# Optimization experiments

Measured on AMD Instinct MI355X. Metric: run time of the kernel, lower is better.

## Reference

```python
import jax, jax.numpy as jnp
import numpy as np

D_MODEL = 768
NUM_HEADS = 12
D_HEAD = D_MODEL // NUM_HEADS
LN_EPS = 1e-5


def layer_norm(x, w, b):
    m = jnp.mean(x, axis=-1, keepdims=True)
    v = jnp.mean(jnp.square(x - m), axis=-1, keepdims=True)
    return (x - m) * jax.lax.rsqrt(v + LN_EPS) * w + b


def setup_inputs() -> dict:
    key = jax.random.key(0)
    ks = jax.random.split(key, 10)
    B, P, NQ, D = 16, 197, 8, D_MODEL
    s = 1.0 / np.sqrt(D)
    return {
        "q_x": jax.random.normal(ks[0], (1, NQ, D), jnp.float32),
        "kv_x": jax.random.normal(ks[1], (B, P, D), jnp.float32),
        "pair_pos_embedding": jax.random.normal(ks[2], (2 * P, D), jnp.float32) * 0.02,
        "q_w": jax.random.normal(ks[3], (D, D), jnp.float32) * s,
        "q_b": jnp.zeros((D,), jnp.float32),
        "kv_w": jax.random.normal(ks[4], (D, D), jnp.float32) * s,
        "kv_b": jnp.zeros((D,), jnp.float32),
        "out_w": jax.random.normal(ks[5], (D, D), jnp.float32) * s,
        "out_b": jnp.zeros((D,), jnp.float32),
        "lnq_w": jnp.ones((D,), jnp.float32),
        "lnq_b": jnp.zeros((D,), jnp.float32),
        "lnkv_w": jnp.ones((D,), jnp.float32),
        "lnkv_b": jnp.zeros((D,), jnp.float32),
    }


def reference(q_x, kv_x, pair_pos_embedding, q_w, q_b, kv_w, kv_b,
              out_w, out_b, lnq_w, lnq_b, lnkv_w, lnkv_b):
    H, dh = NUM_HEADS, D_HEAD
    scale = dh ** -0.5
    _, NQ, D = q_x.shape
    B, P, _ = kv_x.shape

    # q path: Linear -> LN -> split heads -> [1, H, NQ, dh]
    q = layer_norm(q_x @ q_w.T + q_b, lnq_w, lnq_b)
    q = q.reshape(1, NQ, H, dh).transpose(0, 2, 1, 3)  # [1,H,NQ,dh]

    # kv path: Linear -> LN -> split heads -> [B, H, P, dh]
    kv = layer_norm(kv_x @ kv_w.T + kv_b, lnkv_w, lnkv_b)
    kv = kv.reshape(B, P, H, dh).transpose(0, 2, 1, 3)  # [B,H,P,dh]

    # pairwise expansion: kv_concat[i*B+j] = cat(kv[i], kv[j]) along token dim
    kv_rep = jnp.repeat(kv, B, axis=0)          # [B^2,H,P,dh] (repeat_interleave)
    kv_til = jnp.tile(kv, (B, 1, 1, 1))         # [B^2,H,P,dh]
    kv_cat = jnp.concatenate([kv_rep, kv_til], axis=2)  # [B^2,H,2P,dh]

    # positional bias: [2P, D] -> [1, H, 2P, dh]
    pos = pair_pos_embedding.reshape(1, 2 * P, H, dh).transpose(0, 2, 1, 3)
    kv_cat = kv_cat + pos

    scores = jnp.einsum('bhqd,bhpd->bhqp', jnp.broadcast_to(q, (B * B, H, NQ, dh)), kv_cat) * scale
    attn = jax.nn.softmax(scores, axis=-1)      # [B^2,H,NQ,2P]

    v1 = jnp.einsum('bhqp,bhpd->bhqd', attn[..., :P], kv_cat[:, :, :P, :])
    v2 = jnp.einsum('bhqp,bhpd->bhqd', attn[..., P:], kv_cat[:, :, P:, :])
    values = (v1 - v2).transpose(0, 2, 1, 3).reshape(B * B, NQ, D)
    return values @ out_w.T + out_b
```

## Files before the change

kernel.cpp:

```cpp
#include <hip/hip_runtime.h>
#include <hip/hip_bf16.h>
#include <math.h>

#define D_MODEL 768
#define NHEADS  12
#define DHEAD   64
#define NQR     8
#define BB      16
#define PP      197
#define NPAIR   256
#define MKV     (BB*PP)
#define LN_EPSF 1e-5f
#define SCALEF  0.125f

#define KTOT  2304
#define KSPLIT 3
#define KPER  (KTOT/KSPLIT)
#define MPAD  3200
#define BM 128
#define BN 128
#define BK 64

typedef __attribute__((ext_vector_type(8))) short short8v;
typedef __attribute__((ext_vector_type(4))) float float4v;

__device__ __forceinline__ void gload16(const void* g, void* l){
  __builtin_amdgcn_global_load_lds(
      (const __attribute__((address_space(1))) unsigned int*)g,
      (__attribute__((address_space(3))) unsigned int*)l, 16, 0, 0);
}

__global__ __launch_bounds__(256) void qgemm_kernel(
    const float* __restrict__ qx, const float* __restrict__ qw,
    float* __restrict__ qy)
{
  __shared__ float xs[NQR*D_MODEL];
  int tid = threadIdx.x;
  for (int e = tid*4; e < NQR*D_MODEL; e += 1024)
    *(float4*)&xs[e] = *(const float4*)&qx[e];
  __syncthreads();
  int col = tid >> 5, lane = tid & 31;
  int c = blockIdx.x*8 + col;
  const float* wr = qw + (size_t)c*D_MODEL;
  float acc[NQR] = {};
  for (int k = lane*4; k < D_MODEL; k += 128){
    float4 w4 = *(const float4*)&wr[k];
    #pragma unroll
    for (int q = 0; q < NQR; q++){
      float4 x4 = *(const float4*)&xs[q*D_MODEL + k];
      acc[q] += x4.x*w4.x + x4.y*w4.y + x4.z*w4.z + x4.w*w4.w;
    }
  }
  #pragma unroll
  for (int q = 0; q < NQR; q++){
    float a = acc[q];
    for (int off = 16; off >= 1; off >>= 1) a += __shfl_xor(a, off, 32);
    if (lane == 0) qy[q*D_MODEL + c] = a;
  }
}

__global__ __launch_bounds__(256) void ln_rows_kernel(
    const float* __restrict__ Y, const float* __restrict__ bias,
    const float* __restrict__ lnw, const float* __restrict__ lnb,
    float* __restrict__ out)
{
  __shared__ float red[256], red2[256];
  int r = blockIdx.x, tid = threadIdx.x;
  const float* yr = Y + (size_t)r*D_MODEL;
  float x0 = yr[tid      ] + bias[tid      ];
  float x1 = yr[tid + 256] + bias[tid + 256];
  float x2 = yr[tid + 512] + bias[tid + 512];
  red[tid] = x0 + x1 + x2; red2[tid] = x0*x0 + x1*x1 + x2*x2;
  __syncthreads();
  for (int st = 128; st > 0; st >>= 1){
    if (tid < st){ red[tid] += red[tid+st]; red2[tid] += red2[tid+st]; }
    __syncthreads();
  }
  float mean = red[0]*(1.f/768.f);
  float var  = red2[0]*(1.f/768.f) - mean*mean;
  float inv  = rsqrtf(var + LN_EPSF);
  float* orow = out + (size_t)r*D_MODEL;
  orow[tid      ] = (x0-mean)*inv*lnw[tid      ] + lnb[tid      ];
  orow[tid + 256] = (x1-mean)*inv*lnw[tid + 256] + lnb[tid + 256];
  orow[tid + 512] = (x2-mean)*inv*lnw[tid + 512] + lnb[tid + 512];
}

__global__ __launch_bounds__(192) void pack_both_kernel(
    const float* __restrict__ kvx, const float* __restrict__ kvw,
    __hip_bfloat16* __restrict__ Ab, __hip_bfloat16* __restrict__ Wb)
{
  int b = blockIdx.x, t = threadIdx.x;
  const float* X; __hip_bfloat16* Y; int valid, mode, m;
  if (b < MPAD){ X = kvx; Y = Ab; valid = MKV;     mode = 0; m = b; }
  else         { X = kvw; Y = Wb; valid = D_MODEL; mode = 1; m = b - MPAD; }
  int k = t*4;
  float4 v = (m < valid) ? *(const float4*)&X[(size_t)m*D_MODEL + k]
                         : make_float4(0.f,0.f,0.f,0.f);
  float xsv[4] = {v.x, v.y, v.z, v.w};
  unsigned short hu[4], lu[4];
  #pragma unroll
  for (int i = 0; i < 4; i++){
    __hip_bfloat16 h = __float2bfloat16(xsv[i]);
    float hf = __bfloat162float(h);
    __hip_bfloat16 l = __float2bfloat16(xsv[i] - hf);
    hu[i] = *(unsigned short*)&h;
    lu[i] = *(unsigned short*)&l;
  }
  ushort4 hv = {hu[0], hu[1], hu[2], hu[3]};
  ushort4 lv = {lu[0], lu[1], lu[2], lu[3]};
  ushort4* row = (ushort4*)(Y + (size_t)m*KTOT);
  int s = k >> 2;
  if (mode == 0){ row[s] = hv; row[s+192] = hv; row[s+384] = lv; }
  else          { row[s] = hv; row[s+192] = lv; row[s+384] = hv; }
}

__global__ __launch_bounds__(256) void gemm_mfma_kernel(
    const __hip_bfloat16* __restrict__ Ab, const __hip_bfloat16* __restrict__ Wb,
    float* __restrict__ Cp)
{
  __shared__ __hip_bfloat16 As[BM*BK];
  __shared__ __hip_bfloat16 Bs[BN*BK];
  int tid = threadIdx.x;
  int wave = tid >> 6, lane = tid & 63;
  int m0 = blockIdx.x*BM, n0 = blockIdx.y*BN, kt = blockIdx.z;
  int wr = wave >> 1, wc = wave & 1;

  float4v acc[4][4];
  #pragma unroll
  for (int i = 0; i < 4; i++)
    #pragma unroll
    for (int j = 0; j < 4; j++)
      acc[i][j] = (float4v){0.f, 0.f, 0.f, 0.f};

  int sbase = wave*256;
  for (int st = 0; st < KPER/BK; ++st){
    int k0 = kt*KPER + st*BK;
    __syncthreads();
    #pragma unroll
    for (int i = 0; i < 4; i++){
      int s  = sbase + i*64 + lane;
      int r  = s >> 3, kg = s & 7;
      int kgg = kg ^ (r & 7);
      gload16(Ab + (size_t)(m0 + r)*KTOT + k0 + kgg*8, (char*)As + (size_t)s*16);
      gload16(Wb + (size_t)(n0 + r)*KTOT + k0 + kgg*8, (char*)Bs + (size_t)s*16);
    }
    __syncthreads();
    #pragma unroll
    for (int ks = 0; ks < 2; ks++){
      int kq = ks*4 + (lane >> 4);
      short8v af[4], bf[4];
      #pragma unroll
      for (int t = 0; t < 4; t++){
        int ar = wr*64 + t*16 + (lane & 15);
        int as_ = ar*8 + (kq ^ (ar & 7));
        af[t] = *(const short8v*)((const char*)As + (size_t)as_*16);
        int br = wc*64 + t*16 + (lane & 15);
        int bs_ = br*8 + (kq ^ (br & 7));
        bf[t] = *(const short8v*)((const char*)Bs + (size_t)bs_*16);
      }
      #pragma unroll
      for (int i = 0; i < 4; i++)
        #pragma unroll
        for (int j = 0; j < 4; j++)
          acc[i][j] = __builtin_amdgcn_mfma_f32_16x16x32_bf16(af[i], bf[j], acc[i][j], 0, 0, 0);
    }
  }

  float* C = Cp + (size_t)kt*MKV*D_MODEL;
  #pragma unroll
  for (int i = 0; i < 4; i++){
    int mb = m0 + wr*64 + i*16 + ((lane >> 4) << 2);
    #pragma unroll
    for (int j = 0; j < 4; j++){
      int n = n0 + wc*64 + j*16 + (lane & 15);
      #pragma unroll
      for (int r = 0; r < 4; r++){
        int m = mb + r;
        if (m < MKV) C[(size_t)m*D_MODEL + n] = acc[i][j][r];
      }
    }
  }
}

__global__ __launch_bounds__(256) void ln_rows3_kernel(
    const float* __restrict__ Y0, const float* __restrict__ Y1,
    const float* __restrict__ Y2, const float* __restrict__ bias,
    const float* __restrict__ lnw, const float* __restrict__ lnb,
    float* __restrict__ out)
{
  __shared__ float red[256], red2[256];
  int r = blockIdx.x, tid = threadIdx.x;
  const float* y0 = Y0 + (size_t)r*D_MODEL;
  const float* y1 = Y1 + (size_t)r*D_MODEL;
  const float* y2 = Y2 + (size_t)r*D_MODEL;
  float x0 = y0[tid      ] + y1[tid      ] + y2[tid      ] + bias[tid      ];
  float x1 = y0[tid + 256] + y1[tid + 256] + y2[tid + 256] + bias[tid + 256];
  float x2 = y0[tid + 512] + y1[tid + 512] + y2[tid + 512] + bias[tid + 512];
  red[tid] = x0 + x1 + x2; red2[tid] = x0*x0 + x1*x1 + x2*x2;
  __syncthreads();
  for (int st = 128; st > 0; st >>= 1){
    if (tid < st){ red[tid] += red[tid+st]; red2[tid] += red2[tid+st]; }
    __syncthreads();
  }
  float mean = red[0]*(1.f/768.f);
  float var  = red2[0]*(1.f/768.f) - mean*mean;
  float inv  = rsqrtf(var + LN_EPSF);
  float* orow = out + (size_t)r*D_MODEL;
  orow[tid      ] = (x0-mean)*inv*lnw[tid      ] + lnb[tid      ];
  orow[tid + 256] = (x1-mean)*inv*lnw[tid + 256] + lnb[tid + 256];
  orow[tid + 512] = (x2-mean)*inv*lnw[tid + 512] + lnb[tid + 512];
}

#define ATS 256
#define EPS_ 208
__device__ __forceinline__ int at_idx(int d, int p){
  return d*ATS + ((((p >> 2) ^ (d & 7)) << 2) | (p & 3));
}

__global__ __launch_bounds__(256) void rank_proj_kernel(
    const float* __restrict__ kv_ln, const float* __restrict__ q_ln,
    const float* __restrict__ ppe, const float* __restrict__ ow,
    float* __restrict__ m1O, float* __restrict__ z1O,
    float* __restrict__ m2O, float* __restrict__ z2O,
    float* __restrict__ p1, float* __restrict__ p2)
{
  __shared__ float AT[64*ATS];
  __shared__ float qs[NQR*64];
  __shared__ float E[NQR*EPS_];
  __shared__ float Us[NQR*64];
  int r = blockIdx.x, h = blockIdx.y, half = blockIdx.z;
  int tid = threadIdx.x;

  for (int e = tid; e < NQR*64; e += 256){
    int q = e >> 6, d = e & 63;
    qs[e] = q_ln[q*D_MODEL + h*64 + d];
  }
  for (int e = tid; e < 200*64; e += 256){
    int p = e >> 6, d = e & 63;
    float v = 0.f;
    if (p < PP)
      v = kv_ln[((size_t)(r*PP + p))*D_MODEL + h*64 + d]
        + ppe[((size_t)(half*PP + p))*D_MODEL + h*64 + d];
    AT[at_idx(d, p)] = v;
  }
  __syncthreads();

  int q = tid >> 5, sub = tid & 31;
  float s[7];
  #pragma unroll
  for (int i = 0; i < 7; i++) s[i] = 0.f;
  for (int d = 0; d < 64; d++){
    float qv = qs[q*64 + d];
    #pragma unroll
    for (int i = 0; i < 7; i++){
      int p = sub + 32*i;
      int pc = p < PP ? p : PP-1;
      s[i] += qv * AT[at_idx(d, pc)];
    }
  }
  float mloc = -1e30f;
  #pragma unroll
  for (int i = 0; i < 7; i++){
    int p = sub + 32*i;
    s[i] = (p < PP) ? s[i]*SCALEF : -1e30f;
    mloc = fmaxf(mloc, s[i]);
  }
  for (int off = 16; off >= 1; off >>= 1)
    mloc = fmaxf(mloc, __shfl_xor(mloc, off, 32));
  float zloc = 0.f;
  #pragma unroll
  for (int i = 0; i < 7; i++){
    int p = sub + 32*i;
    float e = __expf(s[i] - mloc);
    if (p < PP){ E[q*EPS_ + p] = e; zloc += e; }
    else if (p < 200){ E[q*EPS_ + p] = 0.f; }
  }
  for (int off = 16; off >= 1; off >>= 1)
    zloc += __shfl_xor(zloc, off, 32);

  int idx = (r*NHEADS + h)*NQR + q;
  if (sub == 0){
    if (half){ m2O[idx] = mloc; z2O[idx] = zloc; }
    else     { m1O[idx] = mloc; z1O[idx] = zloc; }
  }

  float u0 = 0.f, u1 = 0.f;
  int sw = (sub & 7);
  for (int p4 = 0; p4 < 200; p4 += 4){
    float4 e4 = *(const float4*)&E[q*EPS_ + p4];
    int cb = (((p4 >> 2) ^ sw) << 2);
    float4 a0 = *(const float4*)&AT[sub*ATS + cb];
    float4 a1 = *(const float4*)&AT[(sub+32)*ATS + cb];
    u0 += e4.x*a0.x + e4.y*a0.y + e4.z*a0.z + e4.w*a0.w;
    u1 += e4.x*a1.x + e4.y*a1.y + e4.z*a1.z + e4.w*a1.w;
  }
  Us[q*64 + sub]      = u0;
  Us[q*64 + sub + 32] = u1;
  __syncthreads();

  float acc[NQR][3];
  #pragma unroll
  for (int m = 0; m < NQR; m++){ acc[m][0]=0.f; acc[m][1]=0.f; acc[m][2]=0.f; }
  const float* owh = ow + h*64;
  for (int d4 = 0; d4 < 64; d4 += 4){
    float4 w0 = *(const float4*)&owh[(size_t)(tid      )*D_MODEL + d4];
    float4 w1 = *(const float4*)&owh[(size_t)(tid + 256)*D_MODEL + d4];
    float4 w2 = *(const float4*)&owh[(size_t)(tid + 512)*D_MODEL + d4];
    #pragma unroll
    for (int m = 0; m < NQR; m++){
      float4 u = *(const float4*)&Us[m*64 + d4];
      acc[m][0] += u.x*w0.x + u.y*w0.y + u.z*w0.z + u.w*w0.w;
      acc[m][1] += u.x*w1.x + u.y*w1.y + u.z*w1.z + u.w*w1.w;
      acc[m][2] += u.x*w2.x + u.y*w2.y + u.z*w2.z + u.w*w2.w;
    }
  }
  float* P = half ? p2 : p1;
  #pragma unroll
  for (int m = 0; m < NQR; m++){
    size_t base = (((size_t)r*NHEADS + h)*NQR + m)*D_MODEL;
    #pragma unroll
    for (int j = 0; j < 3; j++)
      P[base + tid + 256*j] = acc[m][j];
  }
}

__global__ __launch_bounds__(256) void combine_out_kernel(
    const float* __restrict__ m1, const float* __restrict__ z1,
    const float* __restrict__ m2, const float* __restrict__ z2,
    const float* __restrict__ p1, const float* __restrict__ p2,
    const float* __restrict__ out_b, float* __restrict__ out)
{
  __shared__ float c1s[NHEADS], c2s[NHEADS];
  int pair = blockIdx.x, q = blockIdx.y, tid = threadIdx.x;
  int i = pair >> 4, j = pair & 15;
  if (tid < NHEADS){
    int h = tid;
    int ii = (i*NHEADS + h)*NQR + q;
    int jj = (j*NHEADS + h)*NQR + q;
    float mi = m1[ii], mj = m2[jj];
    float mm = fmaxf(mi, mj);
    float a1 = __expf(mi - mm), a2 = __expf(mj - mm);
    float rden = 1.f / (a1*z1[ii] + a2*z2[jj]);
    c1s[h] = a1*rden; c2s[h] = a2*rden;
  }
  __syncthreads();
  float* orow = out + ((size_t)(pair*NQR + q))*D_MODEL;
  for (int nn = tid; nn < D_MODEL; nn += 256){
    float acc = out_b[nn];
    #pragma unroll
    for (int h = 0; h < NHEADS; h++){
      acc += c1s[h]*p1[(((size_t)i*NHEADS + h)*NQR + q)*D_MODEL + nn]
           - c2s[h]*p2[(((size_t)j*NHEADS + h)*NQR + q)*D_MODEL + nn];
    }
    orow[nn] = acc;
  }
}

extern "C" void kernel_launch(void* const* d_in, const int* in_sizes, int n_in,
                              void* d_out, int out_size, void* d_ws, size_t ws_size,
                              hipStream_t stream)
{
  const float* q_x    = (const float*)d_in[0];
  const float* kv_x   = (const float*)d_in[1];
  const float* ppe    = (const float*)d_in[2];
  const float* q_w    = (const float*)d_in[3];
  const float* q_b    = (const float*)d_in[4];
  const float* kv_w   = (const float*)d_in[5];
  const float* kv_b   = (const float*)d_in[6];
  const float* out_w  = (const float*)d_in[7];
  const float* out_b  = (const float*)d_in[8];
  const float* lnq_w  = (const float*)d_in[9];
  const float* lnq_b  = (const float*)d_in[10];
  const float* lnkv_w = (const float*)d_in[11];
  const float* lnkv_b = (const float*)d_in[12];
  float* out = (float*)d_out;

  float* ws    = (float*)d_ws;
  float* q_y   = ws;
  float* q_ln  = q_y  + NQR*D_MODEL;
  float* Abuf_f = q_ln + NQR*D_MODEL;
  float* Wbuf_f = Abuf_f + (size_t)MPAD*KTOT/2;
  float* C0    = Wbuf_f + (size_t)D_MODEL*KTOT/2;
  float* C1    = C0 + (size_t)MKV*D_MODEL;
  float* C2    = C1 + (size_t)MKV*D_MODEL;

  __hip_bfloat16* Abuf = (__hip_bfloat16*)Abuf_f;
  __hip_bfloat16* Wbuf = (__hip_bfloat16*)Wbuf_f;

  float* kv_ln = Abuf_f;
  float* m1    = Wbuf_f;
  float* z1    = m1 + BB*NHEADS*NQR;
  float* m2    = z1 + BB*NHEADS*NQR;
  float* z2    = m2 + BB*NHEADS*NQR;
  float* p1    = C0;
  float* p2    = p1 + (size_t)BB*NHEADS*NQR*D_MODEL;

  qgemm_kernel<<<96, 256, 0, stream>>>(q_x, q_w, q_y);
  ln_rows_kernel<<<NQR, 256, 0, stream>>>(q_y, q_b, lnq_w, lnq_b, q_ln);

  pack_both_kernel<<<MPAD + D_MODEL, 192, 0, stream>>>(kv_x, kv_w, Abuf, Wbuf);

  gemm_mfma_kernel<<<dim3(MPAD/BM, D_MODEL/BN, KSPLIT), 256, 0, stream>>>(
      Abuf, Wbuf, C0);

  ln_rows3_kernel<<<MKV, 256, 0, stream>>>(C0, C1, C2, kv_b, lnkv_w, lnkv_b, kv_ln);

  rank_proj_kernel<<<dim3(BB, NHEADS, 2), 256, 0, stream>>>(
      kv_ln, q_ln, ppe, out_w, m1, z1, m2, z2, p1, p2);

  combine_out_kernel<<<dim3(NPAIR, NQR), 256, 0, stream>>>(
      m1, z1, m2, z2, p1, p2, out_b, out);
}
```

Baseline: 189.2 us.

## Fuse q-path into pack and LN kernels, drop softmax max pass in rank_proj

The q projection GEMM now runs inside the bf16 pack kernel as extra blocks, and the q LayerNorm is folded into the kv LayerNorm kernel. This cuts the launch count from seven to five. rank_proj is restructured to process tokens in two chunks with a padded LDS tile, and it uses wave readlane broadcasts for the exp-weighted value sum. It also drops the max subtraction from the softmax, so the m arrays disappear and combine_out uses a single 1/(z1+z2) factor. Without max stabilisation, exp can overflow if the scaled scores grow large, so correctness relies on LayerNorm keeping the logits small.

```diff
diff --git a/kernel.cpp b/kernel.cpp
--- a/kernel.cpp
+++ b/kernel.cpp
@@ -21,6 +21,10 @@
 #define BN 128
 #define BK 64
 
+#define CH0   100
+#define CH1   97
+#define CHMAX 100
+
 typedef __attribute__((ext_vector_type(8))) short short8v;
 typedef __attribute__((ext_vector_type(4))) float float4v;
 
@@ -30,17 +34,49 @@
       (__attribute__((address_space(3))) unsigned int*)l, 16, 0, 0);
 }
 
-__global__ __launch_bounds__(256) void qgemm_kernel(
+__device__ __forceinline__ float lane_bcast(float v, int src){
+  return __int_as_float(__builtin_amdgcn_readlane(__float_as_int(v), src));
+}
+
+__global__ __launch_bounds__(192) void prep_kernel(
+    const float* __restrict__ kvx, const float* __restrict__ kvw,
+    __hip_bfloat16* __restrict__ Ab, __hip_bfloat16* __restrict__ Wb,
     const float* __restrict__ qx, const float* __restrict__ qw,
     float* __restrict__ qy)
 {
   __shared__ float xs[NQR*D_MODEL];
-  int tid = threadIdx.x;
-  for (int e = tid*4; e < NQR*D_MODEL; e += 1024)
+  int b = blockIdx.x, t = threadIdx.x;
+  if (b < MPAD + D_MODEL){
+    const float* X; __hip_bfloat16* Y; int valid, mode, m;
+    if (b < MPAD){ X = kvx; Y = Ab; valid = MKV;     mode = 0; m = b; }
+    else         { X = kvw; Y = Wb; valid = D_MODEL; mode = 1; m = b - MPAD; }
+    int k = t*4;
+    float4 v = (m < valid) ? *(const float4*)&X[(size_t)m*D_MODEL + k]
+                           : make_float4(0.f,0.f,0.f,0.f);
+    float xsv[4] = {v.x, v.y, v.z, v.w};
+    unsigned short hu[4], lu[4];
+    #pragma unroll
+    for (int i = 0; i < 4; i++){
+      __hip_bfloat16 h = __float2bfloat16(xsv[i]);
+      float hf = __bfloat162float(h);
+      __hip_bfloat16 l = __float2bfloat16(xsv[i] - hf);
+      hu[i] = *(unsigned short*)&h;
+      lu[i] = *(unsigned short*)&l;
+    }
+    ushort4 hv = {hu[0], hu[1], hu[2], hu[3]};
+    ushort4 lv = {lu[0], lu[1], lu[2], lu[3]};
+    ushort4* row = (ushort4*)(Y + (size_t)m*KTOT);
+    int s = k >> 2;
+    if (mode == 0){ row[s] = hv; row[s+192] = hv; row[s+384] = lv; }
+    else          { row[s] = hv; row[s+192] = lv; row[s+384] = hv; }
+    return;
+  }
+  int b2 = b - (MPAD + D_MODEL);
+  for (int e = t*4; e < NQR*D_MODEL; e += 768)
     *(float4*)&xs[e] = *(const float4*)&qx[e];
   __syncthreads();
-  int col = tid >> 5, lane = tid & 31;
-  int c = blockIdx.x*8 + col;
+  int col = t >> 5, lane = t & 31;
+  int c = b2*6 + col;
   const float* wr = qw + (size_t)c*D_MODEL;
   float acc[NQR] = {};
   for (int k = lane*4; k < D_MODEL; k += 128){
@@ -57,61 +93,6 @@
     for (int off = 16; off >= 1; off >>= 1) a += __shfl_xor(a, off, 32);
     if (lane == 0) qy[q*D_MODEL + c] = a;
   }
-}
-
-__global__ __launch_bounds__(256) void ln_rows_kernel(
-    const float* __restrict__ Y, const float* __restrict__ bias,
-    const float* __restrict__ lnw, const float* __restrict__ lnb,
-    float* __restrict__ out)
-{
-  __shared__ float red[256], red2[256];
-  int r = blockIdx.x, tid = threadIdx.x;
-  const float* yr = Y + (size_t)r*D_MODEL;
-  float x0 = yr[tid      ] + bias[tid      ];
-  float x1 = yr[tid + 256] + bias[tid + 256];
-  float x2 = yr[tid + 512] + bias[tid + 512];
-  red[tid] = x0 + x1 + x2; red2[tid] = x0*x0 + x1*x1 + x2*x2;
-  __syncthreads();
-  for (int st = 128; st > 0; st >>= 1){
-    if (tid < st){ red[tid] += red[tid+st]; red2[tid] += red2[tid+st]; }
-    __syncthreads();
-  }
-  float mean = red[0]*(1.f/768.f);
-  float var  = red2[0]*(1.f/768.f) - mean*mean;
-  float inv  = rsqrtf(var + LN_EPSF);
-  float* orow = out + (size_t)r*D_MODEL;
-  orow[tid      ] = (x0-mean)*inv*lnw[tid      ] + lnb[tid      ];
-  orow[tid + 256] = (x1-mean)*inv*lnw[tid + 256] + lnb[tid + 256];
-  orow[tid + 512] = (x2-mean)*inv*lnw[tid + 512] + lnb[tid + 512];
-}
-
-__global__ __launch_bounds__(192) void pack_both_kernel(
-    const float* __restrict__ kvx, const float* __restrict__ kvw,
-    __hip_bfloat16* __restrict__ Ab, __hip_bfloat16* __restrict__ Wb)
-{
-  int b = blockIdx.x, t = threadIdx.x;
-  const float* X; __hip_bfloat16* Y; int valid, mode, m;
-  if (b < MPAD){ X = kvx; Y = Ab; valid = MKV;     mode = 0; m = b; }
-  else         { X = kvw; Y = Wb; valid = D_MODEL; mode = 1; m = b - MPAD; }
-  int k = t*4;
-  float4 v = (m < valid) ? *(const float4*)&X[(size_t)m*D_MODEL + k]
-                         : make_float4(0.f,0.f,0.f,0.f);
-  float xsv[4] = {v.x, v.y, v.z, v.w};
-  unsigned short hu[4], lu[4];
-  #pragma unroll
-  for (int i = 0; i < 4; i++){
-    __hip_bfloat16 h = __float2bfloat16(xsv[i]);
-    float hf = __bfloat162float(h);
-    __hip_bfloat16 l = __float2bfloat16(xsv[i] - hf);
-    hu[i] = *(unsigned short*)&h;
-    lu[i] = *(unsigned short*)&l;
-  }
-  ushort4 hv = {hu[0], hu[1], hu[2], hu[3]};
-  ushort4 lv = {lu[0], lu[1], lu[2], lu[3]};
-  ushort4* row = (ushort4*)(Y + (size_t)m*KTOT);
-  int s = k >> 2;
-  if (mode == 0){ row[s] = hv; row[s+192] = hv; row[s+384] = lv; }
-  else          { row[s] = hv; row[s+192] = lv; row[s+384] = hv; }
 }
 
 __global__ __launch_bounds__(256) void gemm_mfma_kernel(
@@ -182,20 +163,32 @@
   }
 }
 
-__global__ __launch_bounds__(256) void ln_rows3_kernel(
-    const float* __restrict__ Y0, const float* __restrict__ Y1,
-    const float* __restrict__ Y2, const float* __restrict__ bias,
-    const float* __restrict__ lnw, const float* __restrict__ lnb,
-    float* __restrict__ out)
+__global__ __launch_bounds__(256) void ln_all_kernel(
+    const float* __restrict__ C0, const float* __restrict__ C1,
+    const float* __restrict__ C2, const float* __restrict__ kv_b,
+    const float* __restrict__ lnkv_w, const float* __restrict__ lnkv_b,
+    float* __restrict__ kv_ln,
+    const float* __restrict__ q_y, const float* __restrict__ q_b,
+    const float* __restrict__ lnq_w, const float* __restrict__ lnq_b,
+    float* __restrict__ q_ln)
 {
   __shared__ float red[256], red2[256];
-  int r = blockIdx.x, tid = threadIdx.x;
-  const float* y0 = Y0 + (size_t)r*D_MODEL;
-  const float* y1 = Y1 + (size_t)r*D_MODEL;
-  const float* y2 = Y2 + (size_t)r*D_MODEL;
-  float x0 = y0[tid      ] + y1[tid      ] + y2[tid      ] + bias[tid      ];
-  float x1 = y0[tid + 256] + y1[tid + 256] + y2[tid + 256] + bias[tid + 256];
-  float x2 = y0[tid + 512] + y1[tid + 512] + y2[tid + 512] + bias[tid + 512];
+  int b = blockIdx.x, tid = threadIdx.x;
+  const float *xa, *xb, *xc, *bias, *lw, *lb; float* outp; bool three;
+  if (b < MKV){
+    xa = C0 + (size_t)b*D_MODEL; xb = C1 + (size_t)b*D_MODEL;
+    xc = C2 + (size_t)b*D_MODEL;
+    bias = kv_b; lw = lnkv_w; lb = lnkv_b;
+    outp = kv_ln + (size_t)b*D_MODEL; three = true;
+  } else {
+    int r = b - MKV;
+    xa = q_y + (size_t)r*D_MODEL; xb = xa; xc = xa;
+    bias = q_b; lw = lnq_w; lb = lnq_b;
+    outp = q_ln + (size_t)r*D_MODEL; three = false;
+  }
+  float x0 = xa[tid      ] + (three ? xb[tid      ] + xc[tid      ] : 0.f) + bias[tid      ];
+  float x1 = xa[tid + 256] + (three ? xb[tid + 256] + xc[tid + 256] : 0.f) + bias[tid + 256];
+  float x2 = xa[tid + 512] + (three ? xb[tid + 512] + xc[tid + 512] : 0.f) + bias[tid + 512];
   red[tid] = x0 + x1 + x2; red2[tid] = x0*x0 + x1*x1 + x2*x2;
   __syncthreads();
   for (int st = 128; st > 0; st >>= 1){
@@ -205,97 +198,85 @@
   float mean = red[0]*(1.f/768.f);
   float var  = red2[0]*(1.f/768.f) - mean*mean;
   float inv  = rsqrtf(var + LN_EPSF);
-  float* orow = out + (size_t)r*D_MODEL;
-  orow[tid      ] = (x0-mean)*inv*lnw[tid      ] + lnb[tid      ];
-  orow[tid + 256] = (x1-mean)*inv*lnw[tid + 256] + lnb[tid + 256];
-  orow[tid + 512] = (x2-mean)*inv*lnw[tid + 512] + lnb[tid + 512];
-}
-
-#define ATS 256
-#define EPS_ 208
-__device__ __forceinline__ int at_idx(int d, int p){
-  return d*ATS + ((((p >> 2) ^ (d & 7)) << 2) | (p & 3));
+  outp[tid      ] = (x0-mean)*inv*lw[tid      ] + lb[tid      ];
+  outp[tid + 256] = (x1-mean)*inv*lw[tid + 256] + lb[tid + 256];
+  outp[tid + 512] = (x2-mean)*inv*lw[tid + 512] + lb[tid + 512];
 }
 
 __global__ __launch_bounds__(256) void rank_proj_kernel(
     const float* __restrict__ kv_ln, const float* __restrict__ q_ln,
     const float* __restrict__ ppe, const float* __restrict__ ow,
-    float* __restrict__ m1O, float* __restrict__ z1O,
-    float* __restrict__ m2O, float* __restrict__ z2O,
+    float* __restrict__ z1O, float* __restrict__ z2O,
     float* __restrict__ p1, float* __restrict__ p2)
 {
-  __shared__ float AT[64*ATS];
-  __shared__ float qs[NQR*64];
-  __shared__ float E[NQR*EPS_];
+  __shared__ float A[CHMAX*65];
   __shared__ float Us[NQR*64];
   int r = blockIdx.x, h = blockIdx.y, half = blockIdx.z;
   int tid = threadIdx.x;
-
-  for (int e = tid; e < NQR*64; e += 256){
-    int q = e >> 6, d = e & 63;
-    qs[e] = q_ln[q*D_MODEL + h*64 + d];
-  }
-  for (int e = tid; e < 200*64; e += 256){
-    int p = e >> 6, d = e & 63;
-    float v = 0.f;
-    if (p < PP)
-      v = kv_ln[((size_t)(r*PP + p))*D_MODEL + h*64 + d]
-        + ppe[((size_t)(half*PP + p))*D_MODEL + h*64 + d];
-    AT[at_idx(d, p)] = v;
-  }
-  __syncthreads();
-
-  int q = tid >> 5, sub = tid & 31;
-  float s[7];
-  #pragma unroll
-  for (int i = 0; i < 7; i++) s[i] = 0.f;
-  for (int d = 0; d < 64; d++){
-    float qv = qs[q*64 + d];
-    #pragma unroll
-    for (int i = 0; i < 7; i++){
-      int p = sub + 32*i;
-      int pc = p < PP ? p : PP-1;
-      s[i] += qv * AT[at_idx(d, pc)];
-    }
-  }
-  float mloc = -1e30f;
-  #pragma unroll
-  for (int i = 0; i < 7; i++){
-    int p = sub + 32*i;
-    s[i] = (p < PP) ? s[i]*SCALEF : -1e30f;
-    mloc = fmaxf(mloc, s[i]);
-  }
-  for (int off = 16; off >= 1; off >>= 1)
-    mloc = fmaxf(mloc, __shfl_xor(mloc, off, 32));
-  float zloc = 0.f;
-  #pragma unroll
-  for (int i = 0; i < 7; i++){
-    int p = sub + 32*i;
-    float e = __expf(s[i] - mloc);
-    if (p < PP){ E[q*EPS_ + p] = e; zloc += e; }
-    else if (p < 200){ E[q*EPS_ + p] = 0.f; }
-  }
-  for (int off = 16; off >= 1; off >>= 1)
-    zloc += __shfl_xor(zloc, off, 32);
-
-  int idx = (r*NHEADS + h)*NQR + q;
-  if (sub == 0){
-    if (half){ m2O[idx] = mloc; z2O[idx] = zloc; }
-    else     { m1O[idx] = mloc; z1O[idx] = zloc; }
-  }
-
-  float u0 = 0.f, u1 = 0.f;
-  int sw = (sub & 7);
-  for (int p4 = 0; p4 < 200; p4 += 4){
-    float4 e4 = *(const float4*)&E[q*EPS_ + p4];
-    int cb = (((p4 >> 2) ^ sw) << 2);
-    float4 a0 = *(const float4*)&AT[sub*ATS + cb];
-    float4 a1 = *(const float4*)&AT[(sub+32)*ATS + cb];
-    u0 += e4.x*a0.x + e4.y*a0.y + e4.z*a0.z + e4.w*a0.w;
-    u1 += e4.x*a1.x + e4.y*a1.y + e4.z*a1.z + e4.w*a1.w;
-  }
-  Us[q*64 + sub]      = u0;
-  Us[q*64 + sub + 32] = u1;
+  int wave = tid >> 6, lane = tid & 63;
+  int qa = 2*wave, qb = qa + 1;
+  const float* qrowA = q_ln + (size_t)qa*D_MODEL + h*64;
+  const float* qrowB = q_ln + (size_t)qb*D_MODEL + h*64;
+
+  float ua = 0.f, ub = 0.f;
+  float za = 0.f, zb = 0.f;
+
+  for (int c = 0; c < 2; c++){
+    int p0 = c ? CH0 : 0;
+    int np = c ? CH1 : CH0;
+    __syncthreads();
+    for (int e = tid; e < np*16; e += 256){
+      int p = e >> 4, dq = (e & 15) << 2;
+      float4 a = *(const float4*)&kv_ln[((size_t)(r*PP + p0 + p))*D_MODEL + h*64 + dq];
+      float4 b = *(const float4*)&ppe[((size_t)(half*PP + p0 + p))*D_MODEL + h*64 + dq];
+      float* rw = &A[p*65 + dq];
+      rw[0] = a.x + b.x; rw[1] = a.y + b.y;
+      rw[2] = a.z + b.z; rw[3] = a.w + b.w;
+    }
+    __syncthreads();
+
+    int p1v = lane + 64;
+    bool v1 = p1v < np;
+    int p1c = v1 ? p1v : 0;
+    float s0a = 0.f, s0b = 0.f, s1a = 0.f, s1b = 0.f;
+    for (int d = 0; d < 64; d++){
+      float qva = qrowA[d];
+      float qvb = qrowB[d];
+      float a0 = A[lane*65 + d];
+      float a1 = A[p1c*65 + d];
+      s0a += qva*a0; s1a += qva*a1;
+      s0b += qvb*a0; s1b += qvb*a1;
+    }
+    float e0a = __expf(s0a*SCALEF);
+    float e0b = __expf(s0b*SCALEF);
+    float e1a = v1 ? __expf(s1a*SCALEF) : 0.f;
+    float e1b = v1 ? __expf(s1b*SCALEF) : 0.f;
+    za += e0a + e1a;
+    zb += e0b + e1b;
+
+    for (int p = 0; p < 64; p++){
+      float av = A[p*65 + lane];
+      ua += lane_bcast(e0a, p) * av;
+      ub += lane_bcast(e0b, p) * av;
+    }
+    for (int p = 64; p < np; p++){
+      float av = A[p*65 + lane];
+      ua += lane_bcast(e1a, p - 64) * av;
+      ub += lane_bcast(e1b, p - 64) * av;
+    }
+  }
+
+  for (int off = 32; off >= 1; off >>= 1){
+    za += __shfl_xor(za, off);
+    zb += __shfl_xor(zb, off);
+  }
+  float* zO = half ? z2O : z1O;
+  if (lane == 0){
+    zO[(r*NHEADS + h)*NQR + qa] = za;
+    zO[(r*NHEADS + h)*NQR + qb] = zb;
+  }
+  Us[qa*64 + lane] = ua;
+  Us[qb*64 + lane] = ub;
   __syncthreads();
 
   float acc[NQR][3];
@@ -317,31 +298,26 @@
   float* P = half ? p2 : p1;
   #pragma unroll
   for (int m = 0; m < NQR; m++){
-    size_t base = (((size_t)r*NHEADS + h)*NQR + m)*D_MODEL;
+    size_t obase = (((size_t)r*NHEADS + h)*NQR + m)*D_MODEL;
     #pragma unroll
     for (int j = 0; j < 3; j++)
-      P[base + tid + 256*j] = acc[m][j];
+      P[obase + tid + 256*j] = acc[m][j];
   }
 }
 
 __global__ __launch_bounds__(256) void combine_out_kernel(
-    const float* __restrict__ m1, const float* __restrict__ z1,
-    const float* __restrict__ m2, const float* __restrict__ z2,
+    const float* __restrict__ z1, const float* __restrict__ z2,
     const float* __restrict__ p1, const float* __restrict__ p2,
     const float* __restrict__ out_b, float* __restrict__ out)
 {
-  __shared__ float c1s[NHEADS], c2s[NHEADS];
+  __shared__ float cs[NHEADS];
   int pair = blockIdx.x, q = blockIdx.y, tid = threadIdx.x;
   int i = pair >> 4, j = pair & 15;
   if (tid < NHEADS){
     int h = tid;
     int ii = (i*NHEADS + h)*NQR + q;
     int jj = (j*NHEADS + h)*NQR + q;
-    float mi = m1[ii], mj = m2[jj];
-    float mm = fmaxf(mi, mj);
-    float a1 = __expf(mi - mm), a2 = __expf(mj - mm);
-    float rden = 1.f / (a1*z1[ii] + a2*z2[jj]);
-    c1s[h] = a1*rden; c2s[h] = a2*rden;
+    cs[h] = 1.f / (z1[ii] + z2[jj]);
   }
   __syncthreads();
   float* orow = out + ((size_t)(pair*NQR + q))*D_MODEL;
@@ -349,8 +325,8 @@
     float acc = out_b[nn];
     #pragma unroll
     for (int h = 0; h < NHEADS; h++){
-      acc += c1s[h]*p1[(((size_t)i*NHEADS + h)*NQR + q)*D_MODEL + nn]
-           - c2s[h]*p2[(((size_t)j*NHEADS + h)*NQR + q)*D_MODEL + nn];
+      acc += cs[h]*(p1[(((size_t)i*NHEADS + h)*NQR + q)*D_MODEL + nn]
+                  - p2[(((size_t)j*NHEADS + h)*NQR + q)*D_MODEL + nn]);
     }
     orow[nn] = acc;
   }
@@ -388,26 +364,24 @@
   __hip_bfloat16* Wbuf = (__hip_bfloat16*)Wbuf_f;
 
   float* kv_ln = Abuf_f;
-  float* m1    = Wbuf_f;
-  float* z1    = m1 + BB*NHEADS*NQR;
-  float* m2    = z1 + BB*NHEADS*NQR;
-  float* z2    = m2 + BB*NHEADS*NQR;
+  float* z1    = Wbuf_f;
+  float* z2    = z1 + BB*NHEADS*NQR;
   float* p1    = C0;
   float* p2    = p1 + (size_t)BB*NHEADS*NQR*D_MODEL;
 
-  qgemm_kernel<<<96, 256, 0, stream>>>(q_x, q_w, q_y);
-  ln_rows_kernel<<<NQR, 256, 0, stream>>>(q_y, q_b, lnq_w, lnq_b, q_ln);
-
-  pack_both_kernel<<<MPAD + D_MODEL, 192, 0, stream>>>(kv_x, kv_w, Abuf, Wbuf);
+  prep_kernel<<<MPAD + D_MODEL + 128, 192, 0, stream>>>(
+      kv_x, kv_w, Abuf, Wbuf, q_x, q_w, q_y);
 
   gemm_mfma_kernel<<<dim3(MPAD/BM, D_MODEL/BN, KSPLIT), 256, 0, stream>>>(
       Abuf, Wbuf, C0);
 
-  ln_rows3_kernel<<<MKV, 256, 0, stream>>>(C0, C1, C2, kv_b, lnkv_w, lnkv_b, kv_ln);
+  ln_all_kernel<<<MKV + NQR, 256, 0, stream>>>(
+      C0, C1, C2, kv_b, lnkv_w, lnkv_b, kv_ln,
+      q_y, q_b, lnq_w, lnq_b, q_ln);
 
   rank_proj_kernel<<<dim3(BB, NHEADS, 2), 256, 0, stream>>>(
-      kv_ln, q_ln, ppe, out_w, m1, z1, m2, z2, p1, p2);
+      kv_ln, q_ln, ppe, out_w, z1, z2, p1, p2);
 
   combine_out_kernel<<<dim3(NPAIR, NQR), 256, 0, stream>>>(
-      m1, z1, m2, z2, p1, p2, out_b, out);
-}
+      z1, z2, p1, p2, out_b, out);
+}
```

After: 175.4 us. -7.3%, faster.
